# Performance work log

Measured on AMD Instinct MI355X. Metric: run time of the kernel, lower is better.

The kernel has to match this reference:

```python
import jax, jax.numpy as jnp
import numpy as np
from jax.scipy.special import erf

N_GRAPHS, N_PER, C, NB, NEL = 64, 256, 64, 8, 10
DEG = 24
R_MAX = 5.0
P_CUT = 5
AVG_NEIGH = 24.0
SIGMA = 1.0  # atomic_multipoles_smearing_width
L_IDX = jnp.array([0, 1, 1, 1, 2, 2, 2, 2, 2])  # irrep index of each of the 9 sh components


def _sph(v):
    # real spherical harmonics up to l=2, e3nn 'component' normalization, unit input
    x, y, z = v[:, 0], v[:, 1], v[:, 2]
    s3, s15, s5 = 3.0 ** 0.5, 15.0 ** 0.5, 5.0 ** 0.5
    return jnp.stack([
        jnp.ones_like(x),
        s3 * x, s3 * y, s3 * z,
        s15 * x * y, s15 * y * z, 0.5 * s5 * (3.0 * z * z - 1.0),
        s15 * x * z, 0.5 * s15 * (x * x - y * y),
    ], axis=-1)


def _radial(r):
    # Bessel basis * polynomial cutoff envelope (MACE RadialEmbeddingBlock)
    x = r / R_MAX
    p = float(P_CUT)
    env = (1.0 - 0.5 * (p + 1.0) * (p + 2.0) * x ** P_CUT
           + p * (p + 2.0) * x ** (P_CUT + 1)
           - 0.5 * p * (p + 1.0) * x ** (P_CUT + 2))
    env = jnp.where(x < 1.0, env, 0.0)
    n = jnp.arange(1, NB + 1, dtype=r.dtype)
    bess = jnp.sqrt(2.0 / R_MAX) * jnp.sin(n * jnp.pi * x[:, None]) / jnp.clip(r, 1e-9)[:, None]
    return bess * env[:, None]


def setup_inputs() -> dict:
    rng = np.random.default_rng(0)
    N = N_GRAPHS * N_PER
    z = rng.integers(0, NEL, N)
    node_attrs = jnp.asarray(np.eye(NEL, dtype=np.float32)[z])
    pos = rng.uniform(0.0, 8.0, (N, 3)).astype(np.float32)
    positions = jnp.asarray(pos)
    # edges within each graph (no self loops)
    src = rng.integers(0, N_PER, (N_GRAPHS, N_PER * DEG))
    dst = (src + 1 + rng.integers(0, N_PER - 1, (N_GRAPHS, N_PER * DEG))) % N_PER
    off = (np.arange(N_GRAPHS) * N_PER)[:, None]
    edge_index = jnp.asarray(np.stack([(src + off).reshape(-1), (dst + off).reshape(-1)]).astype(np.int64))
    batch = jnp.asarray(np.repeat(np.arange(N_GRAPHS), N_PER).astype(np.int64))
    key = jax.random.key(0)
    ks = jax.random.split(key, 14)
    p = lambda k, shape, s: jax.random.normal(k, shape, jnp.float32) * s
    return dict(
        node_attrs=node_attrs, positions=positions, edge_index=edge_index, batch=batch,
        W_embed=p(ks[0], (NEL, C), 0.3), E0=p(ks[1], (NEL,), 1.0),
        rW1=p(ks[2], (2, NB, 64), 0.3), rW2=p(ks[3], (2, 64, 64), 0.15),
        rW3=p(ks[4], (2, 64, 64), 0.15), rW4=p(ks[5], (2, 64, C), 0.15),
        Wmix=p(ks[6], (2, 3, C, C), 0.1), Wsc=p(ks[7], (2, NEL, C), 0.3),
        w2=p(ks[8], (2, NEL, C), 0.1), w3=p(ks[9], (2, NEL, C), 0.05),
        Wr0=p(ks[10], (C,), 0.1), Wh=p(ks[11], (C, 16), 0.2),
        Wo=p(ks[12], (16,), 0.2), Wq=p(ks[13], (2, C), 0.05),
    )


def reference(node_attrs, positions, edge_index, batch, W_embed, E0, rW1, rW2, rW3, rW4,
              Wmix, Wsc, w2, w3, Wr0, Wh, Wo, Wq):
    N = node_attrs.shape[0]
    src, dst = edge_index[0], edge_index[1]
    # edge vectors / lengths / spherical harmonics / radial features
    vec = positions[dst] - positions[src]                       # [E,3]
    r = jnp.linalg.norm(vec, axis=-1)
    unit = vec / jnp.clip(r, 1e-9)[:, None]
    sh = _sph(unit)                                             # [E,9]
    ef = _radial(r)                                             # [E,NB]
    # node embedding (scalar channel only populated)
    feats = jnp.zeros((N, C, 9), node_attrs.dtype)
    feats = feats.at[:, :, 0].set(node_attrs @ W_embed)
    node_e0 = node_attrs @ E0                                   # [N]
    e0 = jax.ops.segment_sum(node_e0, batch, num_segments=N_GRAPHS)
    energies, node_es = [e0], [node_e0]
    q = jnp.zeros((N,), node_attrs.dtype)
    silu = jax.nn.silu
    for t in range(2):
        # radial MLP -> per-edge, per-channel weights
        R = silu(silu(silu(ef @ rW1[t]) @ rW2[t]) @ rW3[t]) @ rW4[t]   # [E,C]
        s_src = feats[src, :, 0]                                       # [E,C] gather
        msg = (s_src * R)[:, :, None] * sh[:, None, :]                 # [E,C,9]
        agg = jax.ops.segment_sum(msg, dst, num_segments=N) / AVG_NEIGH  # [N,C,9] scatter
        # per-l linear channel mixing
        mixed = jnp.einsum('ncm,mdc->ndm', agg, Wmix[t][L_IDX])        # [N,C,9]
        # correlation-order product basis (element-dependent, up to correlation 3)
        g2 = node_attrs @ w2[t]
        g3 = node_attrs @ w3[t]
        s = mixed[:, :, 0]
        prodf = mixed + (g2 * s)[:, :, None] * mixed + (g3 * s * s)[:, :, None] * mixed
        # element-dependent skip connection
        sc = feats * (node_attrs @ Wsc[t])[:, :, None]
        feats = prodf + sc
        # readout (nonlinear MLP on last layer)
        if t == 1:
            ne = silu(feats[:, :, 0] @ Wh) @ Wo
        else:
            ne = feats[:, :, 0] @ Wr0
        energies.append(jax.ops.segment_sum(ne, batch, num_segments=N_GRAPHS))
        node_es.append(ne)
        # environment-dependent charge source (max_l = 0 -> monopole)
        q = q + feats[:, :, 0] @ Wq[t]
    contributions = jnp.stack(energies, axis=-1)                # [G, L+1]
    total_energy = contributions.sum(-1)
    node_energy = jnp.stack(node_es, axis=-1).sum(-1)
    # direct (PBC-agnostic) Gaussian-smeared Coulomb, per graph
    qg = q.reshape(N_GRAPHS, N_PER)
    pg = positions.reshape(N_GRAPHS, N_PER, 3)
    d = pg[:, :, None, :] - pg[:, None, :, :]
    rij = jnp.sqrt((d * d).sum(-1) + 1e-12)
    ker = erf(rij / (2.0 * SIGMA)) / rij
    ker = jnp.where(jnp.eye(N_PER, dtype=bool)[None], 0.0, ker)  # no self interaction
    ecoul = 0.5 * jnp.einsum('gi,gij,gj->g', qg, ker, qg)
    total_energy = total_energy + ecoul
    dipole = jnp.einsum('gi,gix->gx', qg, pg)                   # [G,3]
    return total_energy, node_energy, contributions, q, dipole
```

## Files before the change

### kernel.cpp

```cpp
#include <hip/hip_runtime.h>
#include <math.h>

#define NGRAPH 64
#define NPER   256
#define NNODE  (NGRAPH*NPER)
#define CDIM   64
#define NELEM  10
#define NEDGE  (NNODE*24)
#define RMAX2  25.0f
#define CE     160

typedef _Float16 half8 __attribute__((ext_vector_type(8)));
typedef float floatx4 __attribute__((ext_vector_type(4)));

__device__ __forceinline__ float silu_f(float x){ return x/(1.f+__expf(-x)); }

__global__ __launch_bounds__(256) void k_pw(
    const float* __restrict__ rW1, const float* __restrict__ rW2,
    const float* __restrict__ rW3, const float* __restrict__ rW4,
    const float* __restrict__ Wmix, _Float16* __restrict__ wH, _Float16* __restrict__ wmixH)
{
  int t = blockIdx.x;
  int tid = threadIdx.x, w = tid>>6, ln = tid&63, ln15 = ln&15, quad = ln>>4;
  const float* Ws[4] = {rW1 + t*512, rW2 + t*4096, rW3 + t*4096, rW4 + t*4096};
  _Float16* wHt    = wH    + (size_t)t*28*512;
  _Float16* wmixHt = wmixH + (size_t)t*24*512;
  for (int f = w; f < 28; f += 4){
    int l, kt, nt;
    if (f < 4){ l = 0; kt = 0; nt = f; }
    else { int g = f-4; l = 1 + g/8; int r8 = g&7; nt = r8>>1; kt = r8&1; }
    const float* Wp = Ws[l];
    half8 v;
    #pragma unroll
    for (int j = 0; j < 8; j++){
      int k = kt*32 + quad*8 + j;
      int c = nt*16 + ln15;
      float x = (l == 0) ? ((k < 8) ? Wp[k*64+c] : 0.f) : Wp[k*64+c];
      v[j] = (_Float16)x;
    }
    *(half8*)&wHt[((size_t)f*64 + ln)*8] = v;
  }
  const float* Wm = Wmix + (size_t)t*3*4096;
  for (int f = w; f < 24; f += 4){
    int l = f>>3, kt = (f>>2)&1, nt = f&3;
    const float* p = Wm + (size_t)l*4096 + (nt*16+ln15)*64 + kt*32 + quad*8;
    half8 v;
    #pragma unroll
    for (int j = 0; j < 8; j++) v[j] = (_Float16)p[j];
    *(half8*)&wmixHt[((size_t)f*64 + ln)*8] = v;
  }
}

__global__ __launch_bounds__(256) void k_prep(
    const float* __restrict__ attrs, const float* __restrict__ E0,
    int* __restrict__ zidx, float* __restrict__ out_ne, float* __restrict__ out_ctr)
{
  __shared__ float red[4];
  int g = blockIdx.x, tid = threadIdx.x, n = g*256 + tid;
  int z = 0;
  #pragma unroll
  for (int k = 1; k < NELEM; k++) if (attrs[n*NELEM+k] > 0.5f) z = k;
  zidx[n] = z;
  float ev = E0[z];
  out_ne[n] = ev;
  float v = ev;
  #pragma unroll
  for (int o = 32; o > 0; o >>= 1) v += __shfl_down(v, o, 64);
  if ((tid&63) == 0) red[tid>>6] = v;
  __syncthreads();
  if (tid == 0) out_ctr[g*3] = red[0]+red[1]+red[2]+red[3];
}

__global__ __launch_bounds__(256) void k_emb(
    const int* __restrict__ zidx, const float* __restrict__ W_embed, _Float16* __restrict__ sH)
{
  int idx = blockIdx.x*256 + threadIdx.x;
  int n = idx >> 6, c = idx & 63;
  sH[idx] = (_Float16)W_embed[zidx[n]*CDIM + c];
}

__global__ __launch_bounds__(256) void k_count(
    const int* __restrict__ ei, const float* __restrict__ pos, int* __restrict__ deg)
{
  int e = blockIdx.x*256 + threadIdx.x;
  int s = ei[e], d = ei[NEDGE+e];
  float vx = pos[d*3]-pos[s*3], vy = pos[d*3+1]-pos[s*3+1], vz = pos[d*3+2]-pos[s*3+2];
  if (vx*vx+vy*vy+vz*vz < RMAX2) atomicAdd(&deg[d], 1);
}

__global__ __launch_bounds__(1024) void k_scan(const int* __restrict__ deg, int* __restrict__ offs)
{
  __shared__ int sums[1024];
  int t = threadIdx.x;
  int loc[16];
  int s = 0, base = t*16;
  #pragma unroll
  for (int i = 0; i < 16; i++){ loc[i] = s; s += deg[base+i]; }
  sums[t] = s;
  __syncthreads();
  for (int off = 1; off < 1024; off <<= 1){
    int v = (t >= off) ? sums[t-off] : 0;
    __syncthreads();
    sums[t] += v;
    __syncthreads();
  }
  int pre = (t > 0) ? sums[t-1] : 0;
  #pragma unroll
  for (int i = 0; i < 16; i++) offs[base+i] = pre + loc[i];
  if (t == 1023) offs[NNODE] = pre + s;
}

__global__ __launch_bounds__(256) void k_fill(
    const int* __restrict__ ei, const float* __restrict__ pos,
    const int* __restrict__ offs, int* __restrict__ cursor,
    int* __restrict__ srcC, _Float16* __restrict__ efH, _Float16* __restrict__ shH)
{
  int e = blockIdx.x*256 + threadIdx.x;
  int s = ei[e], d = ei[NEDGE+e];
  float vx = pos[d*3]-pos[s*3], vy = pos[d*3+1]-pos[s*3+1], vz = pos[d*3+2]-pos[s*3+2];
  float r2 = vx*vx+vy*vy+vz*vz;
  if (r2 >= RMAX2) return;
  int p = atomicAdd(&cursor[d], 1);
  int slot = offs[d] + p;
  srcC[slot] = s;
  float r = sqrtf(r2);
  float inv = 1.f/fmaxf(r, 1e-9f);
  float x_ = vx*inv, y_ = vy*inv, z_ = vz*inv;
  const float s3 = 1.7320508075688772f, s15 = 3.872983346207417f, s5 = 2.2360679774997896f;
  half8 sv0, sv1;
  sv0[0] = (_Float16)1.f;
  sv0[1] = (_Float16)(s3*x_); sv0[2] = (_Float16)(s3*y_); sv0[3] = (_Float16)(s3*z_);
  sv0[4] = (_Float16)(s15*x_*y_); sv0[5] = (_Float16)(s15*y_*z_);
  sv0[6] = (_Float16)(0.5f*s5*(3.f*z_*z_-1.f)); sv0[7] = (_Float16)(s15*x_*z_);
  #pragma unroll
  for (int j = 0; j < 8; j++) sv1[j] = (_Float16)0.f;
  sv1[0] = (_Float16)(0.5f*s15*(x_*x_-y_*y_));
  *(half8*)&shH[(size_t)slot*16]     = sv0;
  *(half8*)&shH[(size_t)slot*16 + 8] = sv1;
  float xx = r*0.2f;
  float x2 = xx*xx;
  float x5 = x2*x2*xx;
  float env = 1.f - 21.f*x5 + 35.f*x5*xx - 15.f*x5*x2;
  float pref = 0.6324555320336759f*inv*env;
  const float PI_ = 3.14159265358979323846f;
  half8 ev, z8;
  #pragma unroll
  for (int b = 0; b < 8; b++) ev[b] = (_Float16)(pref*sinf((float)(b+1)*PI_*xx));
  #pragma unroll
  for (int j = 0; j < 8; j++) z8[j] = (_Float16)0.f;
  _Float16* efp = efH + (size_t)slot*32;
  *(half8*)&efp[0]  = ev;
  *(half8*)&efp[8]  = z8;
  *(half8*)&efp[16] = z8;
  *(half8*)&efp[24] = z8;
}

__global__ __launch_bounds__(256) void k_R(
    const _Float16* __restrict__ efH, const int* __restrict__ srcC,
    const _Float16* __restrict__ sH, const int* __restrict__ nact_p,
    const _Float16* __restrict__ wHt, _Float16* __restrict__ RCh)
{
  __shared__ __align__(16) _Float16 hS[64*72];
  __shared__ int srcS[64];
  int nact = *nact_p;
  int ebase = blockIdx.x*64;
  if (ebase >= nact) return;
  int tid = threadIdx.x;
  int w = tid>>6, ln = tid&63, ln15 = ln&15, quad = ln>>4;

  half8 bL1 = *(const half8*)&wHt[((size_t)(0 + w)*64 + ln)*8];
  half8 bf[3][2];
  #pragma unroll
  for (int l = 0; l < 3; l++){
    bf[l][0] = *(const half8*)&wHt[((size_t)(4 + l*8 + w*2 + 0)*64 + ln)*8];
    bf[l][1] = *(const half8*)&wHt[((size_t)(4 + l*8 + w*2 + 1)*64 + ln)*8];
  }
  if (tid < 64){
    int idx = ebase + tid; if (idx > nact-1) idx = nact-1;
    srcS[tid] = srcC[idx];
  }

  floatx4 zero = {0.f, 0.f, 0.f, 0.f};
  floatx4 acc[4];

  #pragma unroll
  for (int mt = 0; mt < 4; mt++){
    int idx = ebase + mt*16 + ln15; if (idx > nact-1) idx = nact-1;
    half8 a = *(const half8*)&efH[(size_t)idx*32 + quad*8];
    acc[mt] = __builtin_amdgcn_mfma_f32_16x16x32_f16(a, bL1, zero, 0, 0, 0);
  }
  #pragma unroll
  for (int mt = 0; mt < 4; mt++)
    #pragma unroll
    for (int r = 0; r < 4; r++)
      hS[(mt*16 + quad*4 + r)*72 + w*16 + ln15] = (_Float16)silu_f(acc[mt][r]);
  __syncthreads();

  float sv[16];
  #pragma unroll
  for (int mt = 0; mt < 4; mt++)
    #pragma unroll
    for (int r = 0; r < 4; r++){
      int el = mt*16 + quad*4 + r;
      sv[mt*4+r] = (float)sH[(size_t)srcS[el]*64 + w*16 + ln15];
    }

  #pragma unroll
  for (int l = 0; l < 3; l++){
    #pragma unroll
    for (int mt = 0; mt < 4; mt++){
      half8 a0 = *(const half8*)&hS[(mt*16 + ln15)*72 + quad*8];
      half8 a1 = *(const half8*)&hS[(mt*16 + ln15)*72 + 32 + quad*8];
      floatx4 t0 = __builtin_amdgcn_mfma_f32_16x16x32_f16(a0, bf[l][0], zero, 0, 0, 0);
      acc[mt] = __builtin_amdgcn_mfma_f32_16x16x32_f16(a1, bf[l][1], t0, 0, 0, 0);
    }
    __syncthreads();
    if (l < 2){
      #pragma unroll
      for (int mt = 0; mt < 4; mt++)
        #pragma unroll
        for (int r = 0; r < 4; r++)
          hS[(mt*16 + quad*4 + r)*72 + w*16 + ln15] = (_Float16)silu_f(acc[mt][r]);
      __syncthreads();
    }
  }

  #pragma unroll
  for (int mt = 0; mt < 4; mt++)
    #pragma unroll
    for (int r = 0; r < 4; r++){
      int el = mt*16 + quad*4 + r;
      int idx = ebase + el; if (idx > nact-1) idx = nact-1;
      RCh[(size_t)idx*64 + w*16 + ln15] = (_Float16)(acc[mt][r] * sv[mt*4+r]);
    }
}

__global__ __launch_bounds__(256) void k_am(
    const _Float16* __restrict__ RCh, const _Float16* __restrict__ shH,
    const int* __restrict__ offs, const _Float16* __restrict__ sH,
    _Float16* __restrict__ feats1, const _Float16* __restrict__ wmixHt,
    const int* __restrict__ zidx,
    const float* __restrict__ Wsc_t, const float* __restrict__ w2_t,
    const float* __restrict__ w3_t, const float* __restrict__ Wq_t,
    const float* __restrict__ Wr0, const float* __restrict__ Wh, const float* __restrict__ Wo,
    float* __restrict__ out_ne, float* __restrict__ out_ctr, float* __restrict__ out_q, int t)
{
  __shared__ __align__(16) _Float16 uni[CE*80];
  __shared__ _Float16 tabS[1920];
  __shared__ _Float16 WhS[1024];
  __shared__ _Float16 f0S[16*64];
  __shared__ float qS[4][16], neS[4][16];
  __shared__ float WqS[64], Wr0S[64], WoS[16];
  __shared__ int zS[16];
  _Float16* stR = uni;
  _Float16* stS = uni + CE*64;
  _Float16* aggS = uni;

  int blk = blockIdx.x;
  int tid = threadIdx.x;
  int w = tid>>6, ln = tid&63, ln15 = ln&15, quad = ln>>4;

  for (int i = tid; i < 1920; i += 256){
    int t3 = i/640, rem = i - t3*640;
    const float* src = (t3 == 0) ? Wsc_t : (t3 == 1) ? w2_t : w3_t;
    tabS[i] = (_Float16)src[rem];
  }
  for (int i = tid; i < 1024; i += 256) WhS[i] = (_Float16)Wh[i];
  if (tid < 64){ WqS[tid] = Wq_t[tid]; Wr0S[tid] = Wr0[tid]; }
  if (tid < 16){ WoS[tid] = Wo[tid]; zS[tid] = zidx[blk*16+tid]; }

  int beg = offs[blk*16], end = offs[blk*16+16];
  int nb[4], ne_[4];
  #pragma unroll
  for (int i = 0; i < 4; i++){
    nb[i]  = offs[blk*16 + w*4 + i];
    ne_[i] = offs[blk*16 + w*4 + i + 1];
  }

  float acc[4][9];
  #pragma unroll
  for (int i = 0; i < 4; i++)
    #pragma unroll
    for (int m = 0; m < 9; m++) acc[i][m] = 0.f;

  for (int c0 = beg; c0 < end; c0 += CE){
    int ce = end - c0; if (ce > CE) ce = CE;
    __syncthreads();
    for (int i = tid; i < ce*8; i += 256)
      *(half8*)&stR[i*8] = *(const half8*)&RCh[(size_t)c0*64 + i*8];
    for (int i = tid; i < ce*2; i += 256)
      *(half8*)&stS[i*8] = *(const half8*)&shH[(size_t)c0*16 + i*8];
    __syncthreads();
    #pragma unroll
    for (int i = 0; i < 4; i++){
      int pb = nb[i] > c0 ? nb[i] : c0;
      int pe = ne_[i] < c0+ce ? ne_[i] : c0+ce;
      for (int p = pb - c0; p < pe - c0; ++p){
        float rc = (float)stR[p*64 + ln];
        const _Float16* sp = &stS[p*16];
        half8 s0 = *(const half8*)sp;
        float s8 = (float)sp[8];
        acc[i][0] += rc*(float)s0[0]; acc[i][1] += rc*(float)s0[1];
        acc[i][2] += rc*(float)s0[2]; acc[i][3] += rc*(float)s0[3];
        acc[i][4] += rc*(float)s0[4]; acc[i][5] += rc*(float)s0[5];
        acc[i][6] += rc*(float)s0[6]; acc[i][7] += rc*(float)s0[7];
        acc[i][8] += rc*s8;
      }
    }
  }
  __syncthreads();
  #pragma unroll
  for (int i = 0; i < 4; i++){
    int nl = w*4 + i;
    #pragma unroll
    for (int m = 0; m < 9; m++)
      aggS[(m*16 + nl)*72 + ln] = (_Float16)(acc[i][m]*(1.f/24.f));
  }
  __syncthreads();

  floatx4 zero = {0.f, 0.f, 0.f, 0.f};
  floatx4 macc[9];
  #pragma unroll
  for (int m = 0; m < 9; m++){
    int l = (m == 0) ? 0 : ((m < 4) ? 1 : 2);
    half8 a0 = *(const half8*)&aggS[(m*16 + ln15)*72 + quad*8];
    half8 a1 = *(const half8*)&aggS[(m*16 + ln15)*72 + 32 + quad*8];
    half8 b0 = *(const half8*)&wmixHt[((size_t)(l*8 + w)*64 + ln)*8];
    half8 b1 = *(const half8*)&wmixHt[((size_t)(l*8 + 4 + w)*64 + ln)*8];
    floatx4 t0 = __builtin_amdgcn_mfma_f32_16x16x32_f16(a0, b0, zero, 0, 0, 0);
    macc[m] = __builtin_amdgcn_mfma_f32_16x16x32_f16(a1, b1, t0, 0, 0, 0);
  }

  int d = w*16 + ln15;
  #pragma unroll
  for (int r = 0; r < 4; r++){
    int nl = quad*4 + r;
    size_t nglob = (size_t)blk*16 + nl;
    int z = zS[nl];
    float wsc = (float)tabS[z*64+d];
    float g2  = (float)tabS[640 + z*64+d];
    float g3  = (float)tabS[1280 + z*64+d];
    float s0 = macc[0][r];
    float factor = 1.f + g2*s0 + g3*s0*s0;
    float f0 = 0.f;
    #pragma unroll
    for (int m = 0; m < 9; m++){
      float fold;
      if (t == 0) fold = (m == 0) ? (float)sH[nglob*64 + d] : 0.f;
      else        fold = (float)feats1[((size_t)m*NNODE + nglob)*64 + d];
      float fnew = macc[m][r]*factor + fold*wsc;
      if (t == 0) feats1[((size_t)m*NNODE + nglob)*64 + d] = (_Float16)fnew;
      if (m == 0) f0 = fnew;
    }
    if (t == 1) f0S[nl*64 + d] = (_Float16)f0;
    float qv = f0*WqS[d];
    float nev = (t == 0) ? f0*Wr0S[d] : 0.f;
    #pragma unroll
    for (int o = 1; o < 16; o <<= 1){
      qv  += __shfl_xor(qv, o, 16);
      nev += __shfl_xor(nev, o, 16);
    }
    if (ln15 == 0){ qS[w][nl] = qv; neS[w][nl] = nev; }
  }
  __syncthreads();

  if (w == 0 && ln < 16){
    float q = qS[0][ln]+qS[1][ln]+qS[2][ln]+qS[3][ln];
    out_q[blk*16+ln] += q;
    if (t == 0){
      float ne = neS[0][ln]+neS[1][ln]+neS[2][ln]+neS[3][ln];
      out_ne[blk*16+ln] += ne;
      neS[0][ln] = ne;
    }
  }
  if (t == 1 && w == 1){
    int iloc = ln>>4, j = ln&15;
    #pragma unroll
    for (int it = 0; it < 4; it++){
      int i = it*4 + iloc;
      float h = 0.f;
      #pragma unroll 8
      for (int dd = 0; dd < 64; dd++) h += (float)f0S[i*64+dd]*(float)WhS[dd*16+j];
      h = silu_f(h)*WoS[j];
      #pragma unroll
      for (int o = 1; o < 16; o <<= 1) h += __shfl_xor(h, o, 16);
      if (j == 0){ neS[0][i] = h; out_ne[blk*16+i] += h; }
    }
  }
  __syncthreads();
  if (tid == 0){
    float s = 0.f;
    #pragma unroll
    for (int i = 0; i < 16; i++) s += neS[0][i];
    atomicAdd(&out_ctr[(blk>>4)*3 + 1 + t], s);
  }
}

__global__ __launch_bounds__(256) void k_coul(
    const float* __restrict__ q, const float* __restrict__ pos,
    float* __restrict__ te, float* __restrict__ dip)
{
  __shared__ float qs[256], px[256], py[256], pz[256];
  int g = blockIdx.x >> 4, rt = blockIdx.x & 15;
  int tid = threadIdx.x;
  int base = g*256;
  qs[tid] = q[base+tid];
  px[tid] = pos[(base+tid)*3];
  py[tid] = pos[(base+tid)*3+1];
  pz[tid] = pos[(base+tid)*3+2];
  __syncthreads();
  int rloc = rt*16 + (tid>>4);
  int jc = tid & 15;
  float qi = qs[rloc], xi = px[rloc], yi = py[rloc], zi = pz[rloc];
  float srow = 0.f;
  #pragma unroll
  for (int u = 0; u < 16; u++){
    int j = jc*16 + u;
    float dx = xi-px[j], dy = yi-py[j], dz = zi-pz[j];
    float r = sqrtf(dx*dx+dy*dy+dz*dz + 1e-12f);
    float v = erff(0.5f*r)/r;
    srow += (j == rloc) ? 0.f : qs[j]*v;
  }
  #pragma unroll
  for (int o = 8; o > 0; o >>= 1) srow += __shfl_xor(srow, o, 16);
  float vals[4] = {0.f, 0.f, 0.f, 0.f};
  if (jc == 0){ vals[0] = 0.5f*qi*srow; vals[1] = qi*xi; vals[2] = qi*yi; vals[3] = qi*zi; }
  #pragma unroll
  for (int k = 0; k < 4; k++){
    #pragma unroll
    for (int o = 32; o > 0; o >>= 1) vals[k] += __shfl_down(vals[k], o, 64);
  }
  if ((tid&63) == 0){
    atomicAdd(&te[g], vals[0]);
    atomicAdd(&dip[g*3+0], vals[1]);
    atomicAdd(&dip[g*3+1], vals[2]);
    atomicAdd(&dip[g*3+2], vals[3]);
  }
}

__global__ __launch_bounds__(64) void k_fin(const float* __restrict__ ctr, float* __restrict__ te)
{
  int g = threadIdx.x;
  te[g] += ctr[g*3] + ctr[g*3+1] + ctr[g*3+2];
}

extern "C" void kernel_launch(void* const* d_in, const int* in_sizes, int n_in,
                              void* d_out, int out_size, void* d_ws, size_t ws_size,
                              hipStream_t stream)
{
  (void)in_sizes; (void)n_in; (void)out_size; (void)ws_size;
  const float* attrs   = (const float*)d_in[0];
  const float* pos     = (const float*)d_in[1];
  const int*   ei      = (const int*)d_in[2];
  const float* W_embed = (const float*)d_in[4];
  const float* E0      = (const float*)d_in[5];
  const float* rW1     = (const float*)d_in[6];
  const float* rW2     = (const float*)d_in[7];
  const float* rW3     = (const float*)d_in[8];
  const float* rW4     = (const float*)d_in[9];
  const float* Wmix    = (const float*)d_in[10];
  const float* Wsc     = (const float*)d_in[11];
  const float* w2      = (const float*)d_in[12];
  const float* w3      = (const float*)d_in[13];
  const float* Wr0     = (const float*)d_in[14];
  const float* Wh      = (const float*)d_in[15];
  const float* Wo      = (const float*)d_in[16];
  const float* Wq      = (const float*)d_in[17];

  char* base = (char*)d_ws;
  _Float16* efH   = (_Float16*)base; base += (size_t)NEDGE*32*2;
  _Float16* shH   = (_Float16*)base; base += (size_t)NEDGE*16*2;
  _Float16* RCh   = (_Float16*)base; base += (size_t)NEDGE*64*2;
  _Float16* sH    = (_Float16*)base; base += (size_t)NNODE*64*2;
  _Float16* feats1= (_Float16*)base; base += (size_t)9*NNODE*64*2;
  _Float16* wH    = (_Float16*)base; base += (size_t)2*28*512*2;
  _Float16* wmixH = (_Float16*)base; base += (size_t)2*24*512*2;
  int*      deg   = (int*)base;      base += (size_t)NNODE*4;
  int*      offs  = (int*)base;      base += (size_t)(NNODE+1)*4;
  int*      cursor= (int*)base;      base += (size_t)NNODE*4;
  int*      srcC  = (int*)base;      base += (size_t)NEDGE*4;
  int*      zidx  = (int*)base;      base += (size_t)NNODE*4;

  float* out_te  = (float*)d_out;
  float* out_ne  = out_te  + NGRAPH;
  float* out_ctr = out_ne  + NNODE;
  float* out_q   = out_ctr + NGRAPH*3;
  float* out_dip = out_q   + NNODE;

  hipMemsetAsync(d_out, 0, sizeof(float)*(size_t)(NGRAPH + NNODE + NGRAPH*3 + NNODE + NGRAPH*3), stream);
  hipMemsetAsync(deg, 0, sizeof(int)*(size_t)NNODE, stream);
  hipMemsetAsync(cursor, 0, sizeof(int)*(size_t)NNODE, stream);

  k_pw   <<<2, 256, 0, stream>>>(rW1, rW2, rW3, rW4, Wmix, wH, wmixH);
  k_prep <<<NGRAPH, 256, 0, stream>>>(attrs, E0, zidx, out_ne, out_ctr);
  k_emb  <<<NNODE*64/256, 256, 0, stream>>>(zidx, W_embed, sH);
  k_count<<<NEDGE/256, 256, 0, stream>>>(ei, pos, deg);
  k_scan <<<1, 1024, 0, stream>>>(deg, offs);
  k_fill <<<NEDGE/256, 256, 0, stream>>>(ei, pos, offs, cursor, srcC, efH, shH);

  for (int t = 0; t < 2; t++){
    const _Float16* scur = t ? feats1 : sH;
    k_R <<<NEDGE/64, 256, 0, stream>>>(efH, srcC, scur, offs+NNODE,
        wH + (size_t)t*28*512, RCh);
    k_am<<<NNODE/16, 256, 0, stream>>>(RCh, shH, offs, sH, feats1,
        wmixH + (size_t)t*24*512, zidx,
        Wsc + t*NELEM*CDIM, w2 + t*NELEM*CDIM, w3 + t*NELEM*CDIM, Wq + t*CDIM,
        Wr0, Wh, Wo, out_ne, out_ctr, out_q, t);
  }
  k_coul<<<NGRAPH*16, 256, 0, stream>>>(out_q, pos, out_te, out_dip);
  k_fin <<<1, 64, 0, stream>>>(out_ctr, out_te);
}
```

Measured before the change: 295.6 us.

## Fuse the radial MLP into the aggregation kernel and use a sine recurrence

The per-edge radial MLP (k_R) now runs inside the aggregation kernel, on 64-edge chunks of each 16-node block's CSR edge range. The product goes to shared memory instead of a global RCh buffer, which removes one launch per layer and the global write and re-read of the per-edge 64-channel tensor. Separately, the eight Bessel sines in k_fill come from one sincos plus a Chebyshev recurrence instead of eight sinf calls. The cost is more shared-memory use and barriers per chunk, MLP work on the padded tail of each partial chunk, and small fp16 error from the recurrence.

After: 369.9 us. +25.1%, slower.

```diff
diff --git a/kernel.cpp b/kernel.cpp
--- a/kernel.cpp
+++ b/kernel.cpp
@@ -8,7 +8,6 @@
 #define NELEM  10
 #define NEDGE  (NNODE*24)
 #define RMAX2  25.0f
-#define CE     160
 
 typedef _Float16 half8 __attribute__((ext_vector_type(8)));
 typedef float floatx4 __attribute__((ext_vector_type(4)));
@@ -143,9 +142,17 @@
   float env = 1.f - 21.f*x5 + 35.f*x5*xx - 15.f*x5*x2;
   float pref = 0.6324555320336759f*inv*env;
   const float PI_ = 3.14159265358979323846f;
+  float s1, c1;
+  __sincosf(PI_*xx, &s1, &c1);
+  float twoC = 2.f*c1;
+  float sm1 = 0.f, scc = s1;
   half8 ev, z8;
   #pragma unroll
-  for (int b = 0; b < 8; b++) ev[b] = (_Float16)(pref*sinf((float)(b+1)*PI_*xx));
+  for (int b = 0; b < 8; b++){
+    ev[b] = (_Float16)(pref*scc);
+    float nxt = twoC*scc - sm1;
+    sm1 = scc; scc = nxt;
+  }
   #pragma unroll
   for (int j = 0; j < 8; j++) z8[j] = (_Float16)0.f;
   _Float16* efp = efH + (size_t)slot*32;
@@ -155,105 +162,28 @@
   *(half8*)&efp[24] = z8;
 }
 
-__global__ __launch_bounds__(256) void k_R(
+__global__ __launch_bounds__(256) void k_amR(
     const _Float16* __restrict__ efH, const int* __restrict__ srcC,
-    const _Float16* __restrict__ sH, const int* __restrict__ nact_p,
-    const _Float16* __restrict__ wHt, _Float16* __restrict__ RCh)
-{
-  __shared__ __align__(16) _Float16 hS[64*72];
-  __shared__ int srcS[64];
-  int nact = *nact_p;
-  int ebase = blockIdx.x*64;
-  if (ebase >= nact) return;
-  int tid = threadIdx.x;
-  int w = tid>>6, ln = tid&63, ln15 = ln&15, quad = ln>>4;
-
-  half8 bL1 = *(const half8*)&wHt[((size_t)(0 + w)*64 + ln)*8];
-  half8 bf[3][2];
-  #pragma unroll
-  for (int l = 0; l < 3; l++){
-    bf[l][0] = *(const half8*)&wHt[((size_t)(4 + l*8 + w*2 + 0)*64 + ln)*8];
-    bf[l][1] = *(const half8*)&wHt[((size_t)(4 + l*8 + w*2 + 1)*64 + ln)*8];
-  }
-  if (tid < 64){
-    int idx = ebase + tid; if (idx > nact-1) idx = nact-1;
-    srcS[tid] = srcC[idx];
-  }
-
-  floatx4 zero = {0.f, 0.f, 0.f, 0.f};
-  floatx4 acc[4];
-
-  #pragma unroll
-  for (int mt = 0; mt < 4; mt++){
-    int idx = ebase + mt*16 + ln15; if (idx > nact-1) idx = nact-1;
-    half8 a = *(const half8*)&efH[(size_t)idx*32 + quad*8];
-    acc[mt] = __builtin_amdgcn_mfma_f32_16x16x32_f16(a, bL1, zero, 0, 0, 0);
-  }
-  #pragma unroll
-  for (int mt = 0; mt < 4; mt++)
-    #pragma unroll
-    for (int r = 0; r < 4; r++)
-      hS[(mt*16 + quad*4 + r)*72 + w*16 + ln15] = (_Float16)silu_f(acc[mt][r]);
-  __syncthreads();
-
-  float sv[16];
-  #pragma unroll
-  for (int mt = 0; mt < 4; mt++)
-    #pragma unroll
-    for (int r = 0; r < 4; r++){
-      int el = mt*16 + quad*4 + r;
-      sv[mt*4+r] = (float)sH[(size_t)srcS[el]*64 + w*16 + ln15];
-    }
-
-  #pragma unroll
-  for (int l = 0; l < 3; l++){
-    #pragma unroll
-    for (int mt = 0; mt < 4; mt++){
-      half8 a0 = *(const half8*)&hS[(mt*16 + ln15)*72 + quad*8];
-      half8 a1 = *(const half8*)&hS[(mt*16 + ln15)*72 + 32 + quad*8];
-      floatx4 t0 = __builtin_amdgcn_mfma_f32_16x16x32_f16(a0, bf[l][0], zero, 0, 0, 0);
-      acc[mt] = __builtin_amdgcn_mfma_f32_16x16x32_f16(a1, bf[l][1], t0, 0, 0, 0);
-    }
-    __syncthreads();
-    if (l < 2){
-      #pragma unroll
-      for (int mt = 0; mt < 4; mt++)
-        #pragma unroll
-        for (int r = 0; r < 4; r++)
-          hS[(mt*16 + quad*4 + r)*72 + w*16 + ln15] = (_Float16)silu_f(acc[mt][r]);
-      __syncthreads();
-    }
-  }
-
-  #pragma unroll
-  for (int mt = 0; mt < 4; mt++)
-    #pragma unroll
-    for (int r = 0; r < 4; r++){
-      int el = mt*16 + quad*4 + r;
-      int idx = ebase + el; if (idx > nact-1) idx = nact-1;
-      RCh[(size_t)idx*64 + w*16 + ln15] = (_Float16)(acc[mt][r] * sv[mt*4+r]);
-    }
-}
-
-__global__ __launch_bounds__(256) void k_am(
-    const _Float16* __restrict__ RCh, const _Float16* __restrict__ shH,
+    const _Float16* __restrict__ sprev, const _Float16* __restrict__ shH,
     const int* __restrict__ offs, const _Float16* __restrict__ sH,
-    _Float16* __restrict__ feats1, const _Float16* __restrict__ wmixHt,
-    const int* __restrict__ zidx,
+    _Float16* __restrict__ feats1, const _Float16* __restrict__ wHt,
+    const _Float16* __restrict__ wmixHt, const int* __restrict__ zidx,
     const float* __restrict__ Wsc_t, const float* __restrict__ w2_t,
     const float* __restrict__ w3_t, const float* __restrict__ Wq_t,
     const float* __restrict__ Wr0, const float* __restrict__ Wh, const float* __restrict__ Wo,
     float* __restrict__ out_ne, float* __restrict__ out_ctr, float* __restrict__ out_q, int t)
 {
-  __shared__ __align__(16) _Float16 uni[CE*80];
+  __shared__ __align__(16) _Float16 uni[10368];
   __shared__ _Float16 tabS[1920];
   __shared__ _Float16 WhS[1024];
   __shared__ _Float16 f0S[16*64];
   __shared__ float qS[4][16], neS[4][16];
   __shared__ float WqS[64], Wr0S[64], WoS[16];
   __shared__ int zS[16];
-  _Float16* stR = uni;
-  _Float16* stS = uni + CE*64;
+  __shared__ int srcS[64];
+  _Float16* hS   = uni;
+  _Float16* rcS  = uni + 4608;
+  _Float16* shS  = uni + 9216;
   _Float16* aggS = uni;
 
   int blk = blockIdx.x;
@@ -269,6 +199,14 @@
   if (tid < 64){ WqS[tid] = Wq_t[tid]; Wr0S[tid] = Wr0[tid]; }
   if (tid < 16){ WoS[tid] = Wo[tid]; zS[tid] = zidx[blk*16+tid]; }
 
+  half8 bL1 = *(const half8*)&wHt[((size_t)(0 + w)*64 + ln)*8];
+  half8 bf[3][2];
+  #pragma unroll
+  for (int l = 0; l < 3; l++){
+    bf[l][0] = *(const half8*)&wHt[((size_t)(4 + l*8 + w*2 + 0)*64 + ln)*8];
+    bf[l][1] = *(const half8*)&wHt[((size_t)(4 + l*8 + w*2 + 1)*64 + ln)*8];
+  }
+
   int beg = offs[blk*16], end = offs[blk*16+16];
   int nb[4], ne_[4];
   #pragma unroll
@@ -277,34 +215,89 @@
     ne_[i] = offs[blk*16 + w*4 + i + 1];
   }
 
-  float acc[4][9];
+  float accn[4][9];
   #pragma unroll
   for (int i = 0; i < 4; i++)
     #pragma unroll
-    for (int m = 0; m < 9; m++) acc[i][m] = 0.f;
-
-  for (int c0 = beg; c0 < end; c0 += CE){
-    int ce = end - c0; if (ce > CE) ce = CE;
+    for (int m = 0; m < 9; m++) accn[i][m] = 0.f;
+
+  floatx4 zero = {0.f, 0.f, 0.f, 0.f};
+
+  for (int c0 = beg; c0 < end; c0 += 64){
+    int ce = end - c0; if (ce > 64) ce = 64;
     __syncthreads();
-    for (int i = tid; i < ce*8; i += 256)
-      *(half8*)&stR[i*8] = *(const half8*)&RCh[(size_t)c0*64 + i*8];
     for (int i = tid; i < ce*2; i += 256)
-      *(half8*)&stS[i*8] = *(const half8*)&shH[(size_t)c0*16 + i*8];
+      *(half8*)&shS[i*8] = *(const half8*)&shH[(size_t)c0*16 + i*8];
+    if (tid < 64){
+      int idx = c0 + tid; if (idx > end-1) idx = end-1;
+      srcS[tid] = srcC[idx];
+    }
+    floatx4 acc[4];
+    #pragma unroll
+    for (int mt = 0; mt < 4; mt++){
+      int idx = c0 + mt*16 + ln15; if (idx > end-1) idx = end-1;
+      half8 a = *(const half8*)&efH[(size_t)idx*32 + quad*8];
+      acc[mt] = __builtin_amdgcn_mfma_f32_16x16x32_f16(a, bL1, zero, 0, 0, 0);
+    }
+    #pragma unroll
+    for (int mt = 0; mt < 4; mt++)
+      #pragma unroll
+      for (int r = 0; r < 4; r++)
+        hS[(mt*16 + quad*4 + r)*72 + w*16 + ln15] = (_Float16)silu_f(acc[mt][r]);
     __syncthreads();
+
+    float sv[16];
+    #pragma unroll
+    for (int mt = 0; mt < 4; mt++)
+      #pragma unroll
+      for (int r = 0; r < 4; r++){
+        int el = mt*16 + quad*4 + r;
+        sv[mt*4+r] = (float)sprev[(size_t)srcS[el]*64 + w*16 + ln15];
+      }
+
+    #pragma unroll
+    for (int l = 0; l < 3; l++){
+      #pragma unroll
+      for (int mt = 0; mt < 4; mt++){
+        half8 a0 = *(const half8*)&hS[(mt*16 + ln15)*72 + quad*8];
+        half8 a1 = *(const half8*)&hS[(mt*16 + ln15)*72 + 32 + quad*8];
+        floatx4 t0 = __builtin_amdgcn_mfma_f32_16x16x32_f16(a0, bf[l][0], zero, 0, 0, 0);
+        acc[mt] = __builtin_amdgcn_mfma_f32_16x16x32_f16(a1, bf[l][1], t0, 0, 0, 0);
+      }
+      __syncthreads();
+      if (l < 2){
+        #pragma unroll
+        for (int mt = 0; mt < 4; mt++)
+          #pragma unroll
+          for (int r = 0; r < 4; r++)
+            hS[(mt*16 + quad*4 + r)*72 + w*16 + ln15] = (_Float16)silu_f(acc[mt][r]);
+        __syncthreads();
+      }
+    }
+
+    #pragma unroll
+    for (int mt = 0; mt < 4; mt++)
+      #pragma unroll
+      for (int r = 0; r < 4; r++){
+        int el = mt*16 + quad*4 + r;
+        rcS[el*72 + w*16 + ln15] = (_Float16)(acc[mt][r] * sv[mt*4+r]);
+      }
+    __syncthreads();
+
     #pragma unroll
     for (int i = 0; i < 4; i++){
       int pb = nb[i] > c0 ? nb[i] : c0;
       int pe = ne_[i] < c0+ce ? ne_[i] : c0+ce;
       for (int p = pb - c0; p < pe - c0; ++p){
-        float rc = (float)stR[p*64 + ln];
-        const _Float16* sp = &stS[p*16];
+        float rc = (float)rcS[p*72 + ln];
+        const _Float16* sp = &shS[p*16];
         half8 s0 = *(const half8*)sp;
         float s8 = (float)sp[8];
-        acc[i][0] += rc*(float)s0[0]; acc[i][1] += rc*(float)s0[1];
-        acc[i][2] += rc*(float)s0[2]; acc[i][3] += rc*(float)s0[3];
-        acc[i][4] += rc*(float)s0[4]; acc[i][5] += rc*(float)s0[5];
-        acc[i][6] += rc*(float)s0[6]; acc[i][7] += rc*(float)s0[7];
-        acc[i][8] += rc*s8;
+        accn[i][0] += rc*(float)s0[0]; accn[i][1] += rc*(float)s0[1];
+        accn[i][2] += rc*(float)s0[2]; accn[i][3] += rc*(float)s0[3];
+        accn[i][4] += rc*(float)s0[4]; accn[i][5] += rc*(float)s0[5];
+        accn[i][6] += rc*(float)s0[6]; accn[i][7] += rc*(float)s0[7];
+        accn[i][8] += rc*s8;
       }
     }
   }
@@ -314,11 +307,10 @@
     int nl = w*4 + i;
     #pragma unroll
     for (int m = 0; m < 9; m++)
-      aggS[(m*16 + nl)*72 + ln] = (_Float16)(acc[i][m]*(1.f/24.f));
-  }
-  __syncthreads();
-
-  floatx4 zero = {0.f, 0.f, 0.f, 0.f};
+      aggS[(m*16 + nl)*72 + ln] = (_Float16)(accn[i][m]*(1.f/24.f));
+  }
+  __syncthreads();
+
   floatx4 macc[9];
   #pragma unroll
   for (int m = 0; m < 9; m++){
@@ -469,8 +461,7 @@
 
   char* base = (char*)d_ws;
   _Float16* efH   = (_Float16*)base; base += (size_t)NEDGE*32*2;
-  _Float16* shH   = (_Float16*)base; base += (size_t)NEDGE*16*2;
-  _Float16* RCh   = (_Float16*)base; base += (size_t)NEDGE*64*2;
+  _Float16* shH   = (_Float16*)base; base += (size_t)NEDGE*16*2 + 4096;
   _Float16* sH    = (_Float16*)base; base += (size_t)NNODE*64*2;
   _Float16* feats1= (_Float16*)base; base += (size_t)9*NNODE*64*2;
   _Float16* wH    = (_Float16*)base; base += (size_t)2*28*512*2;
@@ -499,11 +490,9 @@
   k_fill <<<NEDGE/256, 256, 0, stream>>>(ei, pos, offs, cursor, srcC, efH, shH);
 
   for (int t = 0; t < 2; t++){
-    const _Float16* scur = t ? feats1 : sH;
-    k_R <<<NEDGE/64, 256, 0, stream>>>(efH, srcC, scur, offs+NNODE,
-        wH + (size_t)t*28*512, RCh);
-    k_am<<<NNODE/16, 256, 0, stream>>>(RCh, shH, offs, sH, feats1,
-        wmixH + (size_t)t*24*512, zidx,
+    const _Float16* sprev = t ? feats1 : sH;
+    k_amR<<<NNODE/16, 256, 0, stream>>>(efH, srcC, sprev, shH, offs, sH, feats1,
+        wH + (size_t)t*28*512, wmixH + (size_t)t*24*512, zidx,
         Wsc + t*NELEM*CDIM, w2 + t*NELEM*CDIM, w3 + t*NELEM*CDIM, Wq + t*CDIM,
         Wr0, Wh, Wo, out_ne, out_ctr, out_q, t);
   }
```

## Halve nodes per aggregation block, shrink LDS staging, use sine recurrence for Bessel basis

Applied to the files above, without the earlier changes.

The aggregation/mixing kernel now handles 8 nodes per block instead of 16, doubling the grid, shrinking the edge staging chunk and dropping the shared Wh copy so more blocks fit per CU (launch bounds hint 5). The MFMA tiles are padded with zero rows for the unused half, which wastes half the matrix work, and the readout reads Wh directly from global memory. Separately, the Bessel basis now uses a Chebyshev sine recurrence from one sincos instead of eight sinf calls, which is cheaper but accumulates slightly more rounding error. A small padding is also added after the shH buffer.

Result: slower. 320.6 us (+8.4%).

```diff
diff --git a/kernel.cpp b/kernel.cpp
--- a/kernel.cpp
+++ b/kernel.cpp
@@ -8,7 +8,7 @@
 #define NELEM  10
 #define NEDGE  (NNODE*24)
 #define RMAX2  25.0f
-#define CE     160
+#define CE     128
 
 typedef _Float16 half8 __attribute__((ext_vector_type(8)));
 typedef float floatx4 __attribute__((ext_vector_type(4)));
@@ -143,9 +143,17 @@
   float env = 1.f - 21.f*x5 + 35.f*x5*xx - 15.f*x5*x2;
   float pref = 0.6324555320336759f*inv*env;
   const float PI_ = 3.14159265358979323846f;
+  float s1, c1;
+  __sincosf(PI_*xx, &s1, &c1);
+  float twoC = 2.f*c1;
+  float sm1 = 0.f, scc = s1;
   half8 ev, z8;
   #pragma unroll
-  for (int b = 0; b < 8; b++) ev[b] = (_Float16)(pref*sinf((float)(b+1)*PI_*xx));
+  for (int b = 0; b < 8; b++){
+    ev[b] = (_Float16)(pref*scc);
+    float nxt = twoC*scc - sm1;
+    sm1 = scc; scc = nxt;
+  }
   #pragma unroll
   for (int j = 0; j < 8; j++) z8[j] = (_Float16)0.f;
   _Float16* efp = efH + (size_t)slot*32;
@@ -235,7 +243,7 @@
     }
 }
 
-__global__ __launch_bounds__(256) void k_am(
+__global__ __launch_bounds__(256, 5) void k_am(
     const _Float16* __restrict__ RCh, const _Float16* __restrict__ shH,
     const int* __restrict__ offs, const _Float16* __restrict__ sH,
     _Float16* __restrict__ feats1, const _Float16* __restrict__ wmixHt,
@@ -247,11 +255,10 @@
 {
   __shared__ __align__(16) _Float16 uni[CE*80];
   __shared__ _Float16 tabS[1920];
-  __shared__ _Float16 WhS[1024];
-  __shared__ _Float16 f0S[16*64];
-  __shared__ float qS[4][16], neS[4][16];
+  __shared__ _Float16 f0S[8*64];
+  __shared__ float qS[4][8], neS[4][8];
   __shared__ float WqS[64], Wr0S[64], WoS[16];
-  __shared__ int zS[16];
+  __shared__ int zS[8];
   _Float16* stR = uni;
   _Float16* stS = uni + CE*64;
   _Float16* aggS = uni;
@@ -265,23 +272,23 @@
     const float* src = (t3 == 0) ? Wsc_t : (t3 == 1) ? w2_t : w3_t;
     tabS[i] = (_Float16)src[rem];
   }
-  for (int i = tid; i < 1024; i += 256) WhS[i] = (_Float16)Wh[i];
   if (tid < 64){ WqS[tid] = Wq_t[tid]; Wr0S[tid] = Wr0[tid]; }
-  if (tid < 16){ WoS[tid] = Wo[tid]; zS[tid] = zidx[blk*16+tid]; }
-
-  int beg = offs[blk*16], end = offs[blk*16+16];
-  int nb[4], ne_[4];
-  #pragma unroll
-  for (int i = 0; i < 4; i++){
-    nb[i]  = offs[blk*16 + w*4 + i];
-    ne_[i] = offs[blk*16 + w*4 + i + 1];
-  }
-
-  float acc[4][9];
-  #pragma unroll
-  for (int i = 0; i < 4; i++)
-    #pragma unroll
-    for (int m = 0; m < 9; m++) acc[i][m] = 0.f;
+  if (tid < 16) WoS[tid] = Wo[tid];
+  if (tid < 8)  zS[tid] = zidx[blk*8+tid];
+
+  int beg = offs[blk*8], end = offs[blk*8+8];
+  int nb[2], ne_[2];
+  #pragma unroll
+  for (int i = 0; i < 2; i++){
+    nb[i]  = offs[blk*8 + w*2 + i];
+    ne_[i] = offs[blk*8 + w*2 + i + 1];
+  }
+
+  float accn[2][9];
+  #pragma unroll
+  for (int i = 0; i < 2; i++)
+    #pragma unroll
+    for (int m = 0; m < 9; m++) accn[i][m] = 0.f;
 
   for (int c0 = beg; c0 < end; c0 += CE){
     int ce = end - c0; if (ce > CE) ce = CE;
@@ -292,7 +299,7 @@
       *(half8*)&stS[i*8] = *(const half8*)&shH[(size_t)c0*16 + i*8];
     __syncthreads();
     #pragma unroll
-    for (int i = 0; i < 4; i++){
+    for (int i = 0; i < 2; i++){
       int pb = nb[i] > c0 ? nb[i] : c0;
       int pe = ne_[i] < c0+ce ? ne_[i] : c0+ce;
       for (int p = pb - c0; p < pe - c0; ++p){
@@ -300,21 +307,21 @@
         const _Float16* sp = &stS[p*16];
         half8 s0 = *(const half8*)sp;
         float s8 = (float)sp[8];
-        acc[i][0] += rc*(float)s0[0]; acc[i][1] += rc*(float)s0[1];
-        acc[i][2] += rc*(float)s0[2]; acc[i][3] += rc*(float)s0[3];
-        acc[i][4] += rc*(float)s0[4]; acc[i][5] += rc*(float)s0[5];
-        acc[i][6] += rc*(float)s0[6]; acc[i][7] += rc*(float)s0[7];
-        acc[i][8] += rc*s8;
+        accn[i][0] += rc*(float)s0[0]; accn[i][1] += rc*(float)s0[1];
+        accn[i][2] += rc*(float)s0[2]; accn[i][3] += rc*(float)s0[3];
+        accn[i][4] += rc*(float)s0[4]; accn[i][5] += rc*(float)s0[5];
+        accn[i][6] += rc*(float)s0[6]; accn[i][7] += rc*(float)s0[7];
+        accn[i][8] += rc*s8;
       }
     }
   }
   __syncthreads();
   #pragma unroll
-  for (int i = 0; i < 4; i++){
-    int nl = w*4 + i;
+  for (int i = 0; i < 2; i++){
+    int nl = w*2 + i;
     #pragma unroll
     for (int m = 0; m < 9; m++)
-      aggS[(m*16 + nl)*72 + ln] = (_Float16)(acc[i][m]*(1.f/24.f));
+      aggS[(m*8 + nl)*72 + ln] = (_Float16)(accn[i][m]*(1.f/24.f));
   }
   __syncthreads();
 
@@ -323,8 +330,14 @@
   #pragma unroll
   for (int m = 0; m < 9; m++){
     int l = (m == 0) ? 0 : ((m < 4) ? 1 : 2);
-    half8 a0 = *(const half8*)&aggS[(m*16 + ln15)*72 + quad*8];
-    half8 a1 = *(const half8*)&aggS[(m*16 + ln15)*72 + 32 + quad*8];
+    half8 a0, a1;
+    if (ln15 < 8){
+      a0 = *(const half8*)&aggS[(m*8 + ln15)*72 + quad*8];
+      a1 = *(const half8*)&aggS[(m*8 + ln15)*72 + 32 + quad*8];
+    } else {
+      #pragma unroll
+      for (int j = 0; j < 8; j++){ a0[j] = (_Float16)0.f; a1[j] = (_Float16)0.f; }
+    }
     half8 b0 = *(const half8*)&wmixHt[((size_t)(l*8 + w)*64 + ln)*8];
     half8 b1 = *(const half8*)&wmixHt[((size_t)(l*8 + 4 + w)*64 + ln)*8];
     floatx4 t0 = __builtin_amdgcn_mfma_f32_16x16x32_f16(a0, b0, zero, 0, 0, 0);
@@ -335,64 +348,66 @@
   #pragma unroll
   for (int r = 0; r < 4; r++){
     int nl = quad*4 + r;
-    size_t nglob = (size_t)blk*16 + nl;
-    int z = zS[nl];
-    float wsc = (float)tabS[z*64+d];
-    float g2  = (float)tabS[640 + z*64+d];
-    float g3  = (float)tabS[1280 + z*64+d];
-    float s0 = macc[0][r];
-    float factor = 1.f + g2*s0 + g3*s0*s0;
-    float f0 = 0.f;
-    #pragma unroll
-    for (int m = 0; m < 9; m++){
-      float fold;
-      if (t == 0) fold = (m == 0) ? (float)sH[nglob*64 + d] : 0.f;
-      else        fold = (float)feats1[((size_t)m*NNODE + nglob)*64 + d];
-      float fnew = macc[m][r]*factor + fold*wsc;
-      if (t == 0) feats1[((size_t)m*NNODE + nglob)*64 + d] = (_Float16)fnew;
-      if (m == 0) f0 = fnew;
-    }
-    if (t == 1) f0S[nl*64 + d] = (_Float16)f0;
-    float qv = f0*WqS[d];
-    float nev = (t == 0) ? f0*Wr0S[d] : 0.f;
-    #pragma unroll
-    for (int o = 1; o < 16; o <<= 1){
-      qv  += __shfl_xor(qv, o, 16);
-      nev += __shfl_xor(nev, o, 16);
-    }
-    if (ln15 == 0){ qS[w][nl] = qv; neS[w][nl] = nev; }
-  }
-  __syncthreads();
-
-  if (w == 0 && ln < 16){
+    if (nl < 8){
+      size_t nglob = (size_t)blk*8 + nl;
+      int z = zS[nl];
+      float wsc = (float)tabS[z*64+d];
+      float g2  = (float)tabS[640 + z*64+d];
+      float g3  = (float)tabS[1280 + z*64+d];
+      float s0 = macc[0][r];
+      float factor = 1.f + g2*s0 + g3*s0*s0;
+      float f0 = 0.f;
+      #pragma unroll
+      for (int m = 0; m < 9; m++){
+        float fold;
+        if (t == 0) fold = (m == 0) ? (float)sH[nglob*64 + d] : 0.f;
+        else        fold = (float)feats1[((size_t)m*NNODE + nglob)*64 + d];
+        float fnew = macc[m][r]*factor + fold*wsc;
+        if (t == 0) feats1[((size_t)m*NNODE + nglob)*64 + d] = (_Float16)fnew;
+        if (m == 0) f0 = fnew;
+      }
+      if (t == 1) f0S[nl*64 + d] = (_Float16)f0;
+      float qv = f0*WqS[d];
+      float nev = (t == 0) ? f0*Wr0S[d] : 0.f;
+      #pragma unroll
+      for (int o = 1; o < 16; o <<= 1){
+        qv  += __shfl_xor(qv, o, 16);
+        nev += __shfl_xor(nev, o, 16);
+      }
+      if (ln15 == 0){ qS[w][nl] = qv; neS[w][nl] = nev; }
+    }
+  }
+  __syncthreads();
+
+  if (w == 0 && ln < 8){
     float q = qS[0][ln]+qS[1][ln]+qS[2][ln]+qS[3][ln];
-    out_q[blk*16+ln] += q;
+    out_q[blk*8+ln] += q;
     if (t == 0){
       float ne = neS[0][ln]+neS[1][ln]+neS[2][ln]+neS[3][ln];
-      out_ne[blk*16+ln] += ne;
+      out_ne[blk*8+ln] += ne;
       neS[0][ln] = ne;
     }
   }
   if (t == 1 && w == 1){
     int iloc = ln>>4, j = ln&15;
     #pragma unroll
-    for (int it = 0; it < 4; it++){
+    for (int it = 0; it < 2; it++){
       int i = it*4 + iloc;
       float h = 0.f;
       #pragma unroll 8
-      for (int dd = 0; dd < 64; dd++) h += (float)f0S[i*64+dd]*(float)WhS[dd*16+j];
+      for (int dd = 0; dd < 64; dd++) h += (float)f0S[i*64+dd]*Wh[dd*16+j];
       h = silu_f(h)*WoS[j];
       #pragma unroll
       for (int o = 1; o < 16; o <<= 1) h += __shfl_xor(h, o, 16);
-      if (j == 0){ neS[0][i] = h; out_ne[blk*16+i] += h; }
+      if (j == 0){ neS[0][i] = h; out_ne[blk*8+i] += h; }
     }
   }
   __syncthreads();
   if (tid == 0){
     float s = 0.f;
     #pragma unroll
-    for (int i = 0; i < 16; i++) s += neS[0][i];
-    atomicAdd(&out_ctr[(blk>>4)*3 + 1 + t], s);
+    for (int i = 0; i < 8; i++) s += neS[0][i];
+    atomicAdd(&out_ctr[(blk>>5)*3 + 1 + t], s);
   }
 }
 
@@ -469,7 +484,7 @@
 
   char* base = (char*)d_ws;
   _Float16* efH   = (_Float16*)base; base += (size_t)NEDGE*32*2;
-  _Float16* shH   = (_Float16*)base; base += (size_t)NEDGE*16*2;
+  _Float16* shH   = (_Float16*)base; base += (size_t)NEDGE*16*2 + 4096;
   _Float16* RCh   = (_Float16*)base; base += (size_t)NEDGE*64*2;
   _Float16* sH    = (_Float16*)base; base += (size_t)NNODE*64*2;
   _Float16* feats1= (_Float16*)base; base += (size_t)9*NNODE*64*2;
@@ -499,10 +514,10 @@
   k_fill <<<NEDGE/256, 256, 0, stream>>>(ei, pos, offs, cursor, srcC, efH, shH);
 
   for (int t = 0; t < 2; t++){
-    const _Float16* scur = t ? feats1 : sH;
-    k_R <<<NEDGE/64, 256, 0, stream>>>(efH, srcC, scur, offs+NNODE,
+    const _Float16* sprev = t ? feats1 : sH;
+    k_R <<<NEDGE/64, 256, 0, stream>>>(efH, srcC, sprev, offs+NNODE,
         wH + (size_t)t*28*512, RCh);
-    k_am<<<NNODE/16, 256, 0, stream>>>(RCh, shH, offs, sH, feats1,
+    k_am<<<NNODE/8, 256, 0, stream>>>(RCh, shH, offs, sH, feats1,
         wmixH + (size_t)t*24*512, zidx,
         Wsc + t*NELEM*CDIM, w2 + t*NELEM*CDIM, w3 + t*NELEM*CDIM, Wq + t*CDIM,
         Wr0, Wh, Wo, out_ne, out_ctr, out_q, t);
```
